# Kernel tuning notes

Measured on AMD Instinct MI355X. Metric: run time of the kernel, lower is better.

Reference implementation:

```python
import jax, jax.numpy as jnp
import numpy as np

N_NODES = 50000
N_EDGES = 640000
IN_FEATS = 128
HID = 128


def setup_inputs() -> dict:
    key = jax.random.key(0)
    ks = jax.random.split(key, 8)
    x = jax.random.normal(ks[0], (N_NODES, IN_FEATS), dtype=jnp.float32)
    src = jax.random.randint(ks[1], (N_EDGES,), 0, N_NODES, dtype=jnp.int32)
    dst = jax.random.randint(ks[2], (N_EDGES,), 0, N_NODES, dtype=jnp.int32)
    s1 = 1.0 / np.sqrt(IN_FEATS)
    s2 = 1.0 / np.sqrt(HID)
    W1 = jax.random.normal(ks[3], (IN_FEATS, HID), dtype=jnp.float32) * s1
    b1 = jnp.zeros((HID,), dtype=jnp.float32)
    W2 = jax.random.normal(ks[4], (HID, HID), dtype=jnp.float32) * s2
    b2 = jnp.zeros((HID,), dtype=jnp.float32)
    Wr = jax.random.normal(ks[5], (HID, 2), dtype=jnp.float32) * s2
    br = jnp.zeros((2,), dtype=jnp.float32)
    return {"x": x, "src": src, "dst": dst, "W1": W1, "b1": b1,
            "W2": W2, "b2": b2, "Wr": Wr, "br": br}


def _degree_norm(idx, n):
    # D^{-1/2}, with 0 for zero-degree nodes (DGL sets inf -> 0)
    deg = jax.ops.segment_sum(jnp.ones(idx.shape[0], jnp.float32), idx, num_segments=n)
    return jnp.where(deg > 0, jax.lax.rsqrt(jnp.maximum(deg, 1.0)), 0.0)


def _graph_conv(h, W, b, src, dst, norm_out, norm_in, n):
    # DGL GraphConv, norm='both': out = D_in^{-1/2} A D_out^{-1/2} (h W) + b
    hW = (h * norm_out[:, None]) @ W          # [N, hid]
    agg = jax.ops.segment_sum(hW[src], dst, num_segments=n)  # gather+scatter over edges
    return agg * norm_in[:, None] + b


def reference(x, src, dst, W1, b1, W2, b2, Wr, br):
    n = x.shape[0]
    norm_out = _degree_norm(src, n)  # source-side out-degree norm
    norm_in = _degree_norm(dst, n)   # dest-side in-degree norm
    h = jax.nn.relu(_graph_conv(x, W1, b1, src, dst, norm_out, norm_in, n))
    h = jax.nn.relu(_graph_conv(h, W2, b2, src, dst, norm_out, norm_in, n))
    hg = jnp.mean(h, axis=0, keepdims=True)  # [1, hid]
    return hg @ Wr + br                      # [1, 2]
```

## Files before the change

kernel.cpp:

```cpp
#include <hip/hip_runtime.h>
#include <hip/hip_bf16.h>

#define FEAT 128
#define RBITS 13
#define RSIZE 8192
#define NCHUNK 32

typedef __attribute__((ext_vector_type(8))) short short8;
typedef __attribute__((ext_vector_type(4))) short short4v;
typedef __attribute__((ext_vector_type(4))) float f32x4;

__device__ __forceinline__ ushort f2bf(float f) {
    union { float f; unsigned u; } v; v.f = f;
    unsigned u = v.u;
    unsigned r = 0x7fffu + ((u >> 16) & 1u);
    return (ushort)((u + r) >> 16);
}
__device__ __forceinline__ float bf2f(short s) {
    union { unsigned u; float f; } v;
    v.u = ((unsigned)(ushort)s) << 16;
    return v.f;
}

__global__ __launch_bounds__(256)
void hist_kernel(const int* __restrict__ src, const int* __restrict__ dst,
                 unsigned* __restrict__ partial, int E, int CS)
{
    __shared__ unsigned hist[RSIZE];
    const int c = blockIdx.x, p = blockIdx.y, job = blockIdx.z;
    const int* __restrict__ idx = job ? dst : src;
    for (int r = threadIdx.x; r < RSIZE; r += 256) hist[r] = 0;
    __syncthreads();
    const int e0 = c * CS, e1 = min(E, e0 + CS);
    const int eA = e0 + ((e1 - e0) & ~3);
    for (int e = e0 + threadIdx.x * 4; e + 4 <= e1; e += 1024) {
        int4 v = *(const int4*)(idx + e);
        if ((v.x >> RBITS) == p) atomicAdd(&hist[v.x & (RSIZE - 1)], 1u);
        if ((v.y >> RBITS) == p) atomicAdd(&hist[v.y & (RSIZE - 1)], 1u);
        if ((v.z >> RBITS) == p) atomicAdd(&hist[v.z & (RSIZE - 1)], 1u);
        if ((v.w >> RBITS) == p) atomicAdd(&hist[v.w & (RSIZE - 1)], 1u);
    }
    for (int e = eA + threadIdx.x; e < e1; e += 256) {
        int v = idx[e];
        if ((v >> RBITS) == p) atomicAdd(&hist[v & (RSIZE - 1)], 1u);
    }
    __syncthreads();
    unsigned* outp = partial +
        (((size_t)job * gridDim.y + p) * NCHUNK + c) * RSIZE;
    for (int r = threadIdx.x; r < RSIZE; r += 256) outp[r] = hist[r];
}

__global__ __launch_bounds__(256)
void merge_kernel(const unsigned* __restrict__ partialOut, unsigned* __restrict__ partialIn,
                  int* __restrict__ cntIn, float* __restrict__ normOut,
                  float* __restrict__ normIn, int* __restrict__ blockSums, int N)
{
    __shared__ int sh[256];
    const int n = blockIdx.x * 256 + threadIdx.x;
    unsigned off = 0;
    if (n < N) {
        const int p = n >> RBITS, r = n & (RSIZE - 1);
        const size_t base = (size_t)p * NCHUNK * RSIZE + r;
        unsigned so = 0;
#pragma unroll 8
        for (int c = 0; c < NCHUNK; ++c) so += partialOut[base + (size_t)c * RSIZE];
#pragma unroll 8
        for (int c = 0; c < NCHUNK; ++c) {
            size_t i = base + (size_t)c * RSIZE;
            unsigned t = partialIn[i];
            partialIn[i] = off;
            off += t;
        }
        cntIn[n]   = (int)off;
        normIn[n]  = off ? rsqrtf((float)off) : 0.0f;
        normOut[n] = so  ? rsqrtf((float)so)  : 0.0f;
    }
    sh[threadIdx.x] = (int)off;
    __syncthreads();
    for (int o = 128; o > 0; o >>= 1) {
        if (threadIdx.x < o) sh[threadIdx.x] += sh[threadIdx.x + o];
        __syncthreads();
    }
    if (threadIdx.x == 0) blockSums[blockIdx.x] = sh[0];
}

__global__ __launch_bounds__(256)
void rowstart_kernel(const int* __restrict__ cntIn, const int* __restrict__ blockSums,
                     int* __restrict__ rowStart, int N, int NB, int E)
{
    __shared__ int bs[256];
    __shared__ int bse[256];
    __shared__ int sh[256];
    const int t = threadIdx.x;
    int bv = (t < NB) ? blockSums[t] : 0;
    bs[t] = bv;
    __syncthreads();
    for (int off = 1; off < 256; off <<= 1) {
        int u = (t >= off) ? bs[t - off] : 0;
        __syncthreads();
        bs[t] += u;
        __syncthreads();
    }
    bse[t] = bs[t] - bv;
    __syncthreads();

    const int i = blockIdx.x * 256 + t;
    int v = (i < N) ? cntIn[i] : 0;
    sh[t] = v;
    __syncthreads();
    for (int off = 1; off < 256; off <<= 1) {
        int u = (t >= off) ? sh[t - off] : 0;
        __syncthreads();
        sh[t] += u;
        __syncthreads();
    }
    if (i < N) rowStart[i] = bse[blockIdx.x] + sh[t] - v;
    if (blockIdx.x == 0 && t == 0) rowStart[N] = E;
}

__global__ __launch_bounds__(256)
void fill_kernel(const int* __restrict__ src, const int* __restrict__ dst,
                 const int* __restrict__ rowStart, const unsigned* __restrict__ chunkOff,
                 int* __restrict__ csrSrc, int N, int E, int CS)
{
    __shared__ unsigned cursor[RSIZE];
    const int c = blockIdx.x, p = blockIdx.y;
    const unsigned* co = chunkOff + ((size_t)p * NCHUNK + c) * RSIZE;
    for (int r = threadIdx.x; r < RSIZE; r += 256) {
        int n = (p << RBITS) + r;
        cursor[r] = (n < N) ? (unsigned)rowStart[n] + co[r] : 0u;
    }
    __syncthreads();
    const int e0 = c * CS, e1 = min(E, e0 + CS);
    const int eA = e0 + ((e1 - e0) & ~3);
    for (int e = e0 + threadIdx.x * 4; e + 4 <= e1; e += 1024) {
        int4 d = *(const int4*)(dst + e);
        if ((d.x >> RBITS) == p) { unsigned q = atomicAdd(&cursor[d.x & (RSIZE - 1)], 1u); csrSrc[q] = src[e]; }
        if ((d.y >> RBITS) == p) { unsigned q = atomicAdd(&cursor[d.y & (RSIZE - 1)], 1u); csrSrc[q] = src[e + 1]; }
        if ((d.z >> RBITS) == p) { unsigned q = atomicAdd(&cursor[d.z & (RSIZE - 1)], 1u); csrSrc[q] = src[e + 2]; }
        if ((d.w >> RBITS) == p) { unsigned q = atomicAdd(&cursor[d.w & (RSIZE - 1)], 1u); csrSrc[q] = src[e + 3]; }
    }
    for (int e = eA + threadIdx.x; e < e1; e += 256) {
        int d = dst[e];
        if ((d >> RBITS) == p) { unsigned q = atomicAdd(&cursor[d & (RSIZE - 1)], 1u); csrSrc[q] = src[e]; }
    }
}

template<bool F32IN>
__global__ __launch_bounds__(256)
void gemm_mfma_kernel(const void* __restrict__ Ain, const float* __restrict__ W,
                      const float* __restrict__ scale, ushort* __restrict__ C,
                      int M, int nStrips)
{
    __shared__ ushort WT[128 * 132];
    __shared__ ushort As[64 * 132];
    __shared__ float  sScale[64];

    const int tid  = threadIdx.x;
    const int wv   = tid >> 6;
    const int lane = tid & 63;
    const int rowHalf = wv >> 1;
    const int colHalf = wv & 1;
    const int l15  = lane & 15;
    const int quad = lane >> 4;

    for (int it = 0; it < 16; ++it) {
        int fid = tid + (it << 8);
        int k   = fid >> 5;
        int c4  = (fid & 31) << 2;
        float4 w = *(const float4*)(W + (size_t)k * FEAT + c4);
        WT[(c4 + 0) * 132 + k] = f2bf(w.x);
        WT[(c4 + 1) * 132 + k] = f2bf(w.y);
        WT[(c4 + 2) * 132 + k] = f2bf(w.z);
        WT[(c4 + 3) * 132 + k] = f2bf(w.w);
    }
    __syncthreads();

    short8 bfrag[4][4];
#pragma unroll
    for (int ct = 0; ct < 4; ++ct) {
        int col = colHalf * 64 + ct * 16 + l15;
#pragma unroll
        for (int kst = 0; kst < 4; ++kst) {
            int k = kst * 32 + quad * 8;
            short4v lo = *(const short4v*)&WT[col * 132 + k];
            short4v hi = *(const short4v*)&WT[col * 132 + k + 4];
            bfrag[ct][kst] = __builtin_shufflevector(lo, hi, 0, 1, 2, 3, 4, 5, 6, 7);
        }
    }

    for (int s = blockIdx.x; s < nStrips; s += gridDim.x) {
        const int row0 = s << 6;
        __syncthreads();

#pragma unroll
        for (int it = 0; it < 4; ++it) {
            int fid = tid + (it << 8);
            int r   = fid >> 4;
            int seg = (fid & 15) << 3;
            int grow = row0 + r;
            short4v lo = {0, 0, 0, 0}, hi = {0, 0, 0, 0};
            if (grow < M) {
                if (F32IN) {
                    const float* pa = (const float*)Ain + (size_t)grow * FEAT + seg;
                    float4 u0 = *(const float4*)(pa);
                    float4 u1 = *(const float4*)(pa + 4);
                    lo[0] = (short)f2bf(u0.x); lo[1] = (short)f2bf(u0.y);
                    lo[2] = (short)f2bf(u0.z); lo[3] = (short)f2bf(u0.w);
                    hi[0] = (short)f2bf(u1.x); hi[1] = (short)f2bf(u1.y);
                    hi[2] = (short)f2bf(u1.z); hi[3] = (short)f2bf(u1.w);
                } else {
                    const ushort* pa = (const ushort*)Ain + (size_t)grow * FEAT + seg;
                    lo = *(const short4v*)(pa);
                    hi = *(const short4v*)(pa + 4);
                }
            }
            *(short4v*)&As[r * 132 + seg]     = lo;
            *(short4v*)&As[r * 132 + seg + 4] = hi;
        }
        if (tid < 64) {
            int grow = row0 + tid;
            sScale[tid] = (grow < M) ? scale[grow] : 0.0f;
        }
        __syncthreads();

        f32x4 acc[2][4] = {};
#pragma unroll
        for (int kst = 0; kst < 4; ++kst) {
            int k = kst * 32 + quad * 8;
            short8 af[2];
#pragma unroll
            for (int rt = 0; rt < 2; ++rt) {
                int row = rowHalf * 32 + rt * 16 + l15;
                short4v lo = *(const short4v*)&As[row * 132 + k];
                short4v hi = *(const short4v*)&As[row * 132 + k + 4];
                af[rt] = __builtin_shufflevector(lo, hi, 0, 1, 2, 3, 4, 5, 6, 7);
            }
#pragma unroll
            for (int rt = 0; rt < 2; ++rt)
#pragma unroll
                for (int ct = 0; ct < 4; ++ct)
                    acc[rt][ct] = __builtin_amdgcn_mfma_f32_16x16x32_bf16(
                        af[rt], bfrag[ct][kst], acc[rt][ct], 0, 0, 0);
        }

#pragma unroll
        for (int rt = 0; rt < 2; ++rt) {
            int rbase = rowHalf * 32 + rt * 16 + quad * 4;
#pragma unroll
            for (int reg = 0; reg < 4; ++reg) {
                int rl = rbase + reg;
                int grow = row0 + rl;
                if (grow < M) {
                    float sc = sScale[rl];
#pragma unroll
                    for (int ct = 0; ct < 4; ++ct) {
                        int col = colHalf * 64 + ct * 16 + l15;
                        C[(size_t)grow * FEAT + col] = f2bf(acc[rt][ct][reg] * sc);
                    }
                }
            }
        }
    }
}

__global__ __launch_bounds__(256)
void gather_kernel(const ushort* __restrict__ t, const int* __restrict__ rowStart,
                   const int* __restrict__ csrSrc, const float* __restrict__ normIn,
                   const float* __restrict__ bias, ushort* __restrict__ out, int N)
{
    const int g    = threadIdx.x >> 5;
    const int lane = threadIdx.x & 31;
    const int h    = lane >> 4;
    const int li   = lane & 15;
    const int node = blockIdx.x * 8 + g;
    if (node >= N) return;
    const int s = rowStart[node];
    const int e = rowStart[node + 1];
    float a[8] = {0.f, 0.f, 0.f, 0.f, 0.f, 0.f, 0.f, 0.f};
    for (int base = s; base < e; base += 32) {
        const int m = min(32, e - base);
        int idx = (base + lane < e) ? csrSrc[base + lane] : 0;
        for (int j0 = 0; j0 < m; j0 += 8) {
            const int jh = j0 + h;
            int s0 = __shfl(idx, jh,     32);
            int s1 = __shfl(idx, jh + 2, 32);
            int s2 = __shfl(idx, jh + 4, 32);
            int s3 = __shfl(idx, jh + 6, 32);
            short8 v0 = {0,0,0,0,0,0,0,0}, v1 = {0,0,0,0,0,0,0,0};
            short8 v2 = {0,0,0,0,0,0,0,0}, v3 = {0,0,0,0,0,0,0,0};
            if (jh     < m) v0 = *(const short8*)(t + (size_t)s0 * FEAT + li * 8);
            if (jh + 2 < m) v1 = *(const short8*)(t + (size_t)s1 * FEAT + li * 8);
            if (jh + 4 < m) v2 = *(const short8*)(t + (size_t)s2 * FEAT + li * 8);
            if (jh + 6 < m) v3 = *(const short8*)(t + (size_t)s3 * FEAT + li * 8);
#pragma unroll
            for (int k = 0; k < 8; ++k)
                a[k] += (bf2f(v0[k]) + bf2f(v1[k])) + (bf2f(v2[k]) + bf2f(v3[k]));
        }
    }
#pragma unroll
    for (int k = 0; k < 8; ++k)
        a[k] += __shfl_xor(a[k], 16, 32);
    if (h == 0) {
        float ni = normIn[node];
        float4 b0 = *(const float4*)(bias + li * 8);
        float4 b1 = *(const float4*)(bias + li * 8 + 4);
        short8 o;
        o[0] = (short)f2bf(fmaxf(fmaf(a[0], ni, b0.x), 0.0f));
        o[1] = (short)f2bf(fmaxf(fmaf(a[1], ni, b0.y), 0.0f));
        o[2] = (short)f2bf(fmaxf(fmaf(a[2], ni, b0.z), 0.0f));
        o[3] = (short)f2bf(fmaxf(fmaf(a[3], ni, b0.w), 0.0f));
        o[4] = (short)f2bf(fmaxf(fmaf(a[4], ni, b1.x), 0.0f));
        o[5] = (short)f2bf(fmaxf(fmaf(a[5], ni, b1.y), 0.0f));
        o[6] = (short)f2bf(fmaxf(fmaf(a[6], ni, b1.z), 0.0f));
        o[7] = (short)f2bf(fmaxf(fmaf(a[7], ni, b1.w), 0.0f));
        *(short8*)(out + (size_t)node * FEAT + li * 8) = o;
    }
}

__global__ __launch_bounds__(256)
void colreduce_kernel(const ushort* __restrict__ h2, float* __restrict__ colsum, int N)
{
    const int c  = threadIdx.x & 127;
    const int rg = threadIdx.x >> 7;
    const int r0 = blockIdx.x * 256;
    const int rEnd = min(r0 + 256, N);
    float acc = 0.0f;
    for (int r = r0 + rg; r < rEnd; r += 2)
        acc += bf2f(h2[(size_t)r * FEAT + c]);
    __shared__ float sh[256];
    sh[threadIdx.x] = acc;
    __syncthreads();
    if (rg == 0) unsafeAtomicAdd(&colsum[c], sh[c] + sh[128 + c]);
}

__global__ __launch_bounds__(128)
void final_kernel(const float* __restrict__ colsum, const float* __restrict__ Wr,
                  const float* __restrict__ br, float* __restrict__ out, float invN)
{
    __shared__ float s0[128], s1[128];
    int j = threadIdx.x;
    float hg = colsum[j] * invN;
    s0[j] = hg * Wr[2 * j + 0];
    s1[j] = hg * Wr[2 * j + 1];
    __syncthreads();
    for (int off = 64; off > 0; off >>= 1) {
        if (j < off) { s0[j] += s0[j + off]; s1[j] += s1[j + off]; }
        __syncthreads();
    }
    if (j == 0) {
        out[0] = s0[0] + br[0];
        out[1] = s1[0] + br[1];
    }
}

extern "C" void kernel_launch(void* const* d_in, const int* in_sizes, int n_in,
                              void* d_out, int out_size, void* d_ws, size_t ws_size,
                              hipStream_t stream)
{
    const float* x   = (const float*)d_in[0];
    const int*   src = (const int*)d_in[1];
    const int*   dst = (const int*)d_in[2];
    const float* W1  = (const float*)d_in[3];
    const float* b1  = (const float*)d_in[4];
    const float* W2  = (const float*)d_in[5];
    const float* b2  = (const float*)d_in[6];
    const float* Wr  = (const float*)d_in[7];
    const float* br  = (const float*)d_in[8];
    float* out = (float*)d_out;

    const int N = in_sizes[0] / FEAT;
    const int E = in_sizes[1];
    const int NP = ((N + 255) / 256) * 256;
    const int NB = (N + 255) / 256;
    const int P  = (N + RSIZE - 1) / RSIZE;
    const int CS = (((E + NCHUNK - 1) / NCHUNK) + 3) & ~3;

    char* p = (char*)d_ws;
    unsigned* partial = (unsigned*)p;    p += (size_t)2 * P * NCHUNK * RSIZE * 4;
    float*  colsum    = (float*)p;       p += 256 * 4;
    int*    blockSums = (int*)p;         p += 256 * 4;
    int*    cntIn     = (int*)p;         p += (size_t)NP * 4;
    float*  normOut   = (float*)p;       p += (size_t)NP * 4;
    float*  normIn    = (float*)p;       p += (size_t)NP * 4;
    int*    rowStart  = (int*)p;         p += (size_t)(NP + 64) * 4;
    int*    csrSrc    = (int*)p;         p += (size_t)E * 4;
    ushort* bufT      = (ushort*)p;      p += (size_t)N * FEAT * 2;
    ushort* bufH      = (ushort*)p;      p += (size_t)N * FEAT * 2;

    unsigned* partialOut = partial;
    unsigned* partialIn  = partial + (size_t)P * NCHUNK * RSIZE;

    hipMemsetAsync(colsum, 0, 256 * 4, stream);

    hist_kernel<<<dim3(NCHUNK, P, 2), 256, 0, stream>>>(src, dst, partial, E, CS);
    merge_kernel<<<NB, 256, 0, stream>>>(partialOut, partialIn, cntIn, normOut, normIn, blockSums, N);
    rowstart_kernel<<<NB, 256, 0, stream>>>(cntIn, blockSums, rowStart, N, NB, E);
    fill_kernel<<<dim3(NCHUNK, P), 256, 0, stream>>>(src, dst, rowStart, partialIn, csrSrc, N, E, CS);

    const int nStrips = (N + 63) / 64;
    const int gathBlocks = (N + 7) / 8;

    gemm_mfma_kernel<true><<<256, 256, 0, stream>>>((const void*)x, W1, normOut, bufT, N, nStrips);
    gather_kernel<<<gathBlocks, 256, 0, stream>>>(bufT, rowStart, csrSrc, normIn, b1, bufH, N);

    gemm_mfma_kernel<false><<<256, 256, 0, stream>>>((const void*)bufH, W2, normOut, bufT, N, nStrips);
    gather_kernel<<<gathBlocks, 256, 0, stream>>>(bufT, rowStart, csrSrc, normIn, b2, bufH, N);

    colreduce_kernel<<<NB, 256, 0, stream>>>(bufH, colsum, N);
    final_kernel<<<1, 128, 0, stream>>>(colsum, Wr, br, out, 1.0f / (float)N);
}
```

Before: 248.3 us.

## Fuse layer-1 gather with layer-2 GEMM and layer-2 gather with column reduction

Layer-1 aggregation now writes its ReLU output straight into shared memory, and the same block runs the W2 MFMA GEMM on it, so the bufH round trip and one launch are gone. Layer-2 aggregation accumulates per-column sums in registers and writes per-block partials, which replaces the bf16 h2 write, the colreduce kernel and the memset. The first GEMM now runs one strip per block instead of a grid-stride loop. In exchange, fusedA rebuilds WT from W2 in every block (782 blocks), and its larger shared-memory footprint may lower occupancy for the latency-bound gather phase.

```diff
diff --git a/kernel.cpp b/kernel.cpp
--- a/kernel.cpp
+++ b/kernel.cpp
@@ -146,9 +146,8 @@
     }
 }
 
-template<bool F32IN>
-__global__ __launch_bounds__(256)
-void gemm_mfma_kernel(const void* __restrict__ Ain, const float* __restrict__ W,
+__global__ __launch_bounds__(256)
+void gemm_mfma_kernel(const float* __restrict__ Ain, const float* __restrict__ W,
                       const float* __restrict__ scale, ushort* __restrict__ C,
                       int M, int nStrips)
 {
@@ -201,19 +200,13 @@
             int grow = row0 + r;
             short4v lo = {0, 0, 0, 0}, hi = {0, 0, 0, 0};
             if (grow < M) {
-                if (F32IN) {
-                    const float* pa = (const float*)Ain + (size_t)grow * FEAT + seg;
-                    float4 u0 = *(const float4*)(pa);
-                    float4 u1 = *(const float4*)(pa + 4);
-                    lo[0] = (short)f2bf(u0.x); lo[1] = (short)f2bf(u0.y);
-                    lo[2] = (short)f2bf(u0.z); lo[3] = (short)f2bf(u0.w);
-                    hi[0] = (short)f2bf(u1.x); hi[1] = (short)f2bf(u1.y);
-                    hi[2] = (short)f2bf(u1.z); hi[3] = (short)f2bf(u1.w);
-                } else {
-                    const ushort* pa = (const ushort*)Ain + (size_t)grow * FEAT + seg;
-                    lo = *(const short4v*)(pa);
-                    hi = *(const short4v*)(pa + 4);
-                }
+                const float* pa = Ain + (size_t)grow * FEAT + seg;
+                float4 u0 = *(const float4*)(pa);
+                float4 u1 = *(const float4*)(pa + 4);
+                lo[0] = (short)f2bf(u0.x); lo[1] = (short)f2bf(u0.y);
+                lo[2] = (short)f2bf(u0.z); lo[3] = (short)f2bf(u0.w);
+                hi[0] = (short)f2bf(u1.x); hi[1] = (short)f2bf(u1.y);
+                hi[2] = (short)f2bf(u1.z); hi[3] = (short)f2bf(u1.w);
             }
             *(short4v*)&As[r * 132 + seg]     = lo;
             *(short4v*)&As[r * 132 + seg + 4] = hi;
@@ -265,90 +258,240 @@
 }
 
 __global__ __launch_bounds__(256)
-void gather_kernel(const ushort* __restrict__ t, const int* __restrict__ rowStart,
+void fusedA_kernel(const ushort* __restrict__ t1, const int* __restrict__ rowStart,
                    const int* __restrict__ csrSrc, const float* __restrict__ normIn,
-                   const float* __restrict__ bias, ushort* __restrict__ out, int N)
+                   const float* __restrict__ bias, const float* __restrict__ W,
+                   const float* __restrict__ normOut, ushort* __restrict__ t2, int N)
+{
+    __shared__ ushort WT[128 * 132];
+    __shared__ ushort As[64 * 132];
+    __shared__ float  sScale[64];
+
+    const int tid  = threadIdx.x;
+    const int wv   = tid >> 6;
+    const int lane = tid & 63;
+    const int rowHalf = wv >> 1;
+    const int colHalf = wv & 1;
+    const int l15  = lane & 15;
+    const int quad = lane >> 4;
+    const int row0 = blockIdx.x << 6;
+
+    for (int it = 0; it < 16; ++it) {
+        int fid = tid + (it << 8);
+        int k   = fid >> 5;
+        int c4  = (fid & 31) << 2;
+        float4 w = *(const float4*)(W + (size_t)k * FEAT + c4);
+        WT[(c4 + 0) * 132 + k] = f2bf(w.x);
+        WT[(c4 + 1) * 132 + k] = f2bf(w.y);
+        WT[(c4 + 2) * 132 + k] = f2bf(w.z);
+        WT[(c4 + 3) * 132 + k] = f2bf(w.w);
+    }
+    if (tid < 64) {
+        int grow = row0 + tid;
+        sScale[tid] = (grow < N) ? normOut[grow] : 0.0f;
+    }
+    __syncthreads();
+
+    short8 bfrag[4][4];
+#pragma unroll
+    for (int ct = 0; ct < 4; ++ct) {
+        int col = colHalf * 64 + ct * 16 + l15;
+#pragma unroll
+        for (int kst = 0; kst < 4; ++kst) {
+            int k = kst * 32 + quad * 8;
+            short4v lo = *(const short4v*)&WT[col * 132 + k];
+            short4v hi = *(const short4v*)&WT[col * 132 + k + 4];
+            bfrag[ct][kst] = __builtin_shufflevector(lo, hi, 0, 1, 2, 3, 4, 5, 6, 7);
+        }
+    }
+
+    {
+        const int g    = tid >> 5;
+        const int gl   = tid & 31;
+        const int h    = gl >> 4;
+        const int li   = gl & 15;
+        const float4 b0 = *(const float4*)(bias + li * 8);
+        const float4 b1 = *(const float4*)(bias + li * 8 + 4);
+        for (int i = g; i < 64; i += 8) {
+            const int node = row0 + i;
+            float a[8] = {0.f, 0.f, 0.f, 0.f, 0.f, 0.f, 0.f, 0.f};
+            if (node < N) {
+                const int s = rowStart[node];
+                const int e = rowStart[node + 1];
+                for (int base = s; base < e; base += 32) {
+                    const int m = min(32, e - base);
+                    int idx = (base + gl < e) ? csrSrc[base + gl] : 0;
+                    for (int j0 = 0; j0 < m; j0 += 8) {
+                        const int jh = j0 + h;
+                        int s0 = __shfl(idx, jh,     32);
+                        int s1 = __shfl(idx, jh + 2, 32);
+                        int s2 = __shfl(idx, jh + 4, 32);
+                        int s3 = __shfl(idx, jh + 6, 32);
+                        short8 v0 = {0,0,0,0,0,0,0,0}, v1 = {0,0,0,0,0,0,0,0};
+                        short8 v2 = {0,0,0,0,0,0,0,0}, v3 = {0,0,0,0,0,0,0,0};
+                        if (jh     < m) v0 = *(const short8*)(t1 + (size_t)s0 * FEAT + li * 8);
+                        if (jh + 2 < m) v1 = *(const short8*)(t1 + (size_t)s1 * FEAT + li * 8);
+                        if (jh + 4 < m) v2 = *(const short8*)(t1 + (size_t)s2 * FEAT + li * 8);
+                        if (jh + 6 < m) v3 = *(const short8*)(t1 + (size_t)s3 * FEAT + li * 8);
+#pragma unroll
+                        for (int k = 0; k < 8; ++k)
+                            a[k] += (bf2f(v0[k]) + bf2f(v1[k])) + (bf2f(v2[k]) + bf2f(v3[k]));
+                    }
+                }
+            }
+#pragma unroll
+            for (int k = 0; k < 8; ++k)
+                a[k] += __shfl_xor(a[k], 16, 32);
+            if (h == 0) {
+                short8 o = {0,0,0,0,0,0,0,0};
+                if (node < N) {
+                    float ni = normIn[node];
+                    o[0] = (short)f2bf(fmaxf(fmaf(a[0], ni, b0.x), 0.0f));
+                    o[1] = (short)f2bf(fmaxf(fmaf(a[1], ni, b0.y), 0.0f));
+                    o[2] = (short)f2bf(fmaxf(fmaf(a[2], ni, b0.z), 0.0f));
+                    o[3] = (short)f2bf(fmaxf(fmaf(a[3], ni, b0.w), 0.0f));
+                    o[4] = (short)f2bf(fmaxf(fmaf(a[4], ni, b1.x), 0.0f));
+                    o[5] = (short)f2bf(fmaxf(fmaf(a[5], ni, b1.y), 0.0f));
+                    o[6] = (short)f2bf(fmaxf(fmaf(a[6], ni, b1.z), 0.0f));
+                    o[7] = (short)f2bf(fmaxf(fmaf(a[7], ni, b1.w), 0.0f));
+                }
+                *(short8*)&As[i * 132 + li * 8] = o;
+            }
+        }
+    }
+    __syncthreads();
+
+    f32x4 acc[2][4] = {};
+#pragma unroll
+    for (int kst = 0; kst < 4; ++kst) {
+        int k = kst * 32 + quad * 8;
+        short8 af[2];
+#pragma unroll
+        for (int rt = 0; rt < 2; ++rt) {
+            int row = rowHalf * 32 + rt * 16 + l15;
+            short4v lo = *(const short4v*)&As[row * 132 + k];
+            short4v hi = *(const short4v*)&As[row * 132 + k + 4];
+            af[rt] = __builtin_shufflevector(lo, hi, 0, 1, 2, 3, 4, 5, 6, 7);
+        }
+#pragma unroll
+        for (int rt = 0; rt < 2; ++rt)
+#pragma unroll
+            for (int ct = 0; ct < 4; ++ct)
+                acc[rt][ct] = __builtin_amdgcn_mfma_f32_16x16x32_bf16(
+                    af[rt], bfrag[ct][kst], acc[rt][ct], 0, 0, 0);
+    }
+
+#pragma unroll
+    for (int rt = 0; rt < 2; ++rt) {
+        int rbase = rowHalf * 32 + rt * 16 + quad * 4;
+#pragma unroll
+        for (int reg = 0; reg < 4; ++reg) {
+            int rl = rbase + reg;
+            int grow = row0 + rl;
+            if (grow < N) {
+                float sc = sScale[rl];
+#pragma unroll
+                for (int ct = 0; ct < 4; ++ct) {
+                    int col = colHalf * 64 + ct * 16 + l15;
+                    t2[(size_t)grow * FEAT + col] = f2bf(acc[rt][ct][reg] * sc);
+                }
+            }
+        }
+    }
+}
+
+__global__ __launch_bounds__(256)
+void fusedB_kernel(const ushort* __restrict__ t2, const int* __restrict__ rowStart,
+                   const int* __restrict__ csrSrc, const float* __restrict__ normIn,
+                   const float* __restrict__ bias, float* __restrict__ partials, int N)
 {
     const int g    = threadIdx.x >> 5;
-    const int lane = threadIdx.x & 31;
-    const int h    = lane >> 4;
-    const int li   = lane & 15;
-    const int node = blockIdx.x * 8 + g;
-    if (node >= N) return;
-    const int s = rowStart[node];
-    const int e = rowStart[node + 1];
-    float a[8] = {0.f, 0.f, 0.f, 0.f, 0.f, 0.f, 0.f, 0.f};
-    for (int base = s; base < e; base += 32) {
-        const int m = min(32, e - base);
-        int idx = (base + lane < e) ? csrSrc[base + lane] : 0;
-        for (int j0 = 0; j0 < m; j0 += 8) {
-            const int jh = j0 + h;
-            int s0 = __shfl(idx, jh,     32);
-            int s1 = __shfl(idx, jh + 2, 32);
-            int s2 = __shfl(idx, jh + 4, 32);
-            int s3 = __shfl(idx, jh + 6, 32);
-            short8 v0 = {0,0,0,0,0,0,0,0}, v1 = {0,0,0,0,0,0,0,0};
-            short8 v2 = {0,0,0,0,0,0,0,0}, v3 = {0,0,0,0,0,0,0,0};
-            if (jh     < m) v0 = *(const short8*)(t + (size_t)s0 * FEAT + li * 8);
-            if (jh + 2 < m) v1 = *(const short8*)(t + (size_t)s1 * FEAT + li * 8);
-            if (jh + 4 < m) v2 = *(const short8*)(t + (size_t)s2 * FEAT + li * 8);
-            if (jh + 6 < m) v3 = *(const short8*)(t + (size_t)s3 * FEAT + li * 8);
-#pragma unroll
-            for (int k = 0; k < 8; ++k)
-                a[k] += (bf2f(v0[k]) + bf2f(v1[k])) + (bf2f(v2[k]) + bf2f(v3[k]));
-        }
-    }
-#pragma unroll
-    for (int k = 0; k < 8; ++k)
-        a[k] += __shfl_xor(a[k], 16, 32);
+    const int gl   = threadIdx.x & 31;
+    const int h    = gl >> 4;
+    const int li   = gl & 15;
+    const float4 b0 = *(const float4*)(bias + li * 8);
+    const float4 b1 = *(const float4*)(bias + li * 8 + 4);
+    const int stride = gridDim.x * 8;
+
+    float racc[8] = {0.f, 0.f, 0.f, 0.f, 0.f, 0.f, 0.f, 0.f};
+    for (int node = blockIdx.x * 8 + g; node < N; node += stride) {
+        const int s = rowStart[node];
+        const int e = rowStart[node + 1];
+        float a[8] = {0.f, 0.f, 0.f, 0.f, 0.f, 0.f, 0.f, 0.f};
+        for (int base = s; base < e; base += 32) {
+            const int m = min(32, e - base);
+            int idx = (base + gl < e) ? csrSrc[base + gl] : 0;
+            for (int j0 = 0; j0 < m; j0 += 8) {
+                const int jh = j0 + h;
+                int s0 = __shfl(idx, jh,     32);
+                int s1 = __shfl(idx, jh + 2, 32);
+                int s2 = __shfl(idx, jh + 4, 32);
+                int s3 = __shfl(idx, jh + 6, 32);
+                short8 v0 = {0,0,0,0,0,0,0,0}, v1 = {0,0,0,0,0,0,0,0};
+                short8 v2 = {0,0,0,0,0,0,0,0}, v3 = {0,0,0,0,0,0,0,0};
+                if (jh     < m) v0 = *(const short8*)(t2 + (size_t)s0 * FEAT + li * 8);
+                if (jh + 2 < m) v1 = *(const short8*)(t2 + (size_t)s1 * FEAT + li * 8);
+                if (jh + 4 < m) v2 = *(const short8*)(t2 + (size_t)s2 * FEAT + li * 8);
+                if (jh + 6 < m) v3 = *(const short8*)(t2 + (size_t)s3 * FEAT + li * 8);
+#pragma unroll
+                for (int k = 0; k < 8; ++k)
+                    a[k] += (bf2f(v0[k]) + bf2f(v1[k])) + (bf2f(v2[k]) + bf2f(v3[k]));
+            }
+        }
+#pragma unroll
+        for (int k = 0; k < 8; ++k)
+            a[k] += __shfl_xor(a[k], 16, 32);
+        if (h == 0) {
+            float ni = normIn[node];
+            racc[0] += fmaxf(fmaf(a[0], ni, b0.x), 0.0f);
+            racc[1] += fmaxf(fmaf(a[1], ni, b0.y), 0.0f);
+            racc[2] += fmaxf(fmaf(a[2], ni, b0.z), 0.0f);
+            racc[3] += fmaxf(fmaf(a[3], ni, b0.w), 0.0f);
+            racc[4] += fmaxf(fmaf(a[4], ni, b1.x), 0.0f);
+            racc[5] += fmaxf(fmaf(a[5], ni, b1.y), 0.0f);
+            racc[6] += fmaxf(fmaf(a[6], ni, b1.z), 0.0f);
+            racc[7] += fmaxf(fmaf(a[7], ni, b1.w), 0.0f);
+        }
+    }
+
+    __shared__ float colsh[8][128];
     if (h == 0) {
-        float ni = normIn[node];
-        float4 b0 = *(const float4*)(bias + li * 8);
-        float4 b1 = *(const float4*)(bias + li * 8 + 4);
-        short8 o;
-        o[0] = (short)f2bf(fmaxf(fmaf(a[0], ni, b0.x), 0.0f));
-        o[1] = (short)f2bf(fmaxf(fmaf(a[1], ni, b0.y), 0.0f));
-        o[2] = (short)f2bf(fmaxf(fmaf(a[2], ni, b0.z), 0.0f));
-        o[3] = (short)f2bf(fmaxf(fmaf(a[3], ni, b0.w), 0.0f));
-        o[4] = (short)f2bf(fmaxf(fmaf(a[4], ni, b1.x), 0.0f));
-        o[5] = (short)f2bf(fmaxf(fmaf(a[5], ni, b1.y), 0.0f));
-        o[6] = (short)f2bf(fmaxf(fmaf(a[6], ni, b1.z), 0.0f));
-        o[7] = (short)f2bf(fmaxf(fmaf(a[7], ni, b1.w), 0.0f));
-        *(short8*)(out + (size_t)node * FEAT + li * 8) = o;
-    }
-}
-
-__global__ __launch_bounds__(256)
-void colreduce_kernel(const ushort* __restrict__ h2, float* __restrict__ colsum, int N)
-{
+#pragma unroll
+        for (int k = 0; k < 8; ++k) colsh[g][li * 8 + k] = racc[k];
+    }
+    __syncthreads();
+    if (threadIdx.x < 128) {
+        float sum = 0.f;
+#pragma unroll
+        for (int gg = 0; gg < 8; ++gg) sum += colsh[gg][threadIdx.x];
+        partials[(size_t)blockIdx.x * 128 + threadIdx.x] = sum;
+    }
+}
+
+__global__ __launch_bounds__(512)
+void final_kernel(const float* __restrict__ partials, const float* __restrict__ Wr,
+                  const float* __restrict__ br, float* __restrict__ out, float invN, int G)
+{
+    __shared__ float cs[4][128];
+    __shared__ float s0[128], s1[128];
     const int c  = threadIdx.x & 127;
     const int rg = threadIdx.x >> 7;
-    const int r0 = blockIdx.x * 256;
-    const int rEnd = min(r0 + 256, N);
-    float acc = 0.0f;
-    for (int r = r0 + rg; r < rEnd; r += 2)
-        acc += bf2f(h2[(size_t)r * FEAT + c]);
-    __shared__ float sh[256];
-    sh[threadIdx.x] = acc;
-    __syncthreads();
-    if (rg == 0) unsafeAtomicAdd(&colsum[c], sh[c] + sh[128 + c]);
-}
-
-__global__ __launch_bounds__(128)
-void final_kernel(const float* __restrict__ colsum, const float* __restrict__ Wr,
-                  const float* __restrict__ br, float* __restrict__ out, float invN)
-{
-    __shared__ float s0[128], s1[128];
-    int j = threadIdx.x;
-    float hg = colsum[j] * invN;
-    s0[j] = hg * Wr[2 * j + 0];
-    s1[j] = hg * Wr[2 * j + 1];
+    float acc = 0.f;
+    for (int b = rg; b < G; b += 4)
+        acc += partials[(size_t)b * 128 + c];
+    cs[rg][c] = acc;
+    __syncthreads();
+    if (rg == 0) {
+        float hg = (cs[0][c] + cs[1][c] + cs[2][c] + cs[3][c]) * invN;
+        s0[c] = hg * Wr[2 * c + 0];
+        s1[c] = hg * Wr[2 * c + 1];
+    }
     __syncthreads();
     for (int off = 64; off > 0; off >>= 1) {
-        if (j < off) { s0[j] += s0[j + off]; s1[j] += s1[j + off]; }
-        __syncthreads();
-    }
-    if (j == 0) {
+        if (threadIdx.x < off) { s0[threadIdx.x] += s0[threadIdx.x + off]; s1[threadIdx.x] += s1[threadIdx.x + off]; }
+        __syncthreads();
+    }
+    if (threadIdx.x == 0) {
         out[0] = s0[0] + br[0];
         out[1] = s1[0] + br[1];
     }
@@ -375,23 +518,22 @@
     const int NB = (N + 255) / 256;
     const int P  = (N + RSIZE - 1) / RSIZE;
     const int CS = (((E + NCHUNK - 1) / NCHUNK) + 3) & ~3;
+    const int GB = 1024;
 
     char* p = (char*)d_ws;
     unsigned* partial = (unsigned*)p;    p += (size_t)2 * P * NCHUNK * RSIZE * 4;
-    float*  colsum    = (float*)p;       p += 256 * 4;
     int*    blockSums = (int*)p;         p += 256 * 4;
     int*    cntIn     = (int*)p;         p += (size_t)NP * 4;
     float*  normOut   = (float*)p;       p += (size_t)NP * 4;
     float*  normIn    = (float*)p;       p += (size_t)NP * 4;
     int*    rowStart  = (int*)p;         p += (size_t)(NP + 64) * 4;
     int*    csrSrc    = (int*)p;         p += (size_t)E * 4;
-    ushort* bufT      = (ushort*)p;      p += (size_t)N * FEAT * 2;
-    ushort* bufH      = (ushort*)p;      p += (size_t)N * FEAT * 2;
+    float*  partials  = (float*)p;       p += (size_t)GB * 128 * 4;
+    ushort* bufT1     = (ushort*)p;      p += (size_t)N * FEAT * 2;
+    ushort* bufT2     = (ushort*)p;      p += (size_t)N * FEAT * 2;
 
     unsigned* partialOut = partial;
     unsigned* partialIn  = partial + (size_t)P * NCHUNK * RSIZE;
-
-    hipMemsetAsync(colsum, 0, 256 * 4, stream);
 
     hist_kernel<<<dim3(NCHUNK, P, 2), 256, 0, stream>>>(src, dst, partial, E, CS);
     merge_kernel<<<NB, 256, 0, stream>>>(partialOut, partialIn, cntIn, normOut, normIn, blockSums, N);
@@ -399,14 +541,12 @@
     fill_kernel<<<dim3(NCHUNK, P), 256, 0, stream>>>(src, dst, rowStart, partialIn, csrSrc, N, E, CS);
 
     const int nStrips = (N + 63) / 64;
-    const int gathBlocks = (N + 7) / 8;
-
-    gemm_mfma_kernel<true><<<256, 256, 0, stream>>>((const void*)x, W1, normOut, bufT, N, nStrips);
-    gather_kernel<<<gathBlocks, 256, 0, stream>>>(bufT, rowStart, csrSrc, normIn, b1, bufH, N);
-
-    gemm_mfma_kernel<false><<<256, 256, 0, stream>>>((const void*)bufH, W2, normOut, bufT, N, nStrips);
-    gather_kernel<<<gathBlocks, 256, 0, stream>>>(bufT, rowStart, csrSrc, normIn, b2, bufH, N);
-
-    colreduce_kernel<<<NB, 256, 0, stream>>>(bufH, colsum, N);
-    final_kernel<<<1, 128, 0, stream>>>(colsum, Wr, br, out, 1.0f / (float)N);
-}
+
+    gemm_mfma_kernel<<<nStrips, 256, 0, stream>>>(x, W1, normOut, bufT1, N, nStrips);
+
+    fusedA_kernel<<<nStrips, 256, 0, stream>>>(bufT1, rowStart, csrSrc, normIn, b1, W2, normOut, bufT2, N);
+
+    fusedB_kernel<<<GB, 256, 0, stream>>>(bufT2, rowStart, csrSrc, normIn, b2, partials, N);
+
+    final_kernel<<<1, 512, 0, stream>>>(partials, Wr, br, out, 1.0f / (float)N, GB);
+}
```

After: 278.0 us. 12.0% more time.
